# Optimization experiments

Measured on AMD Instinct MI355X. Metric: run time of the kernel, lower is better.

The kernel has to match this reference:

```python
import jax, jax.numpy as jnp
from jax import lax
import numpy as np

B, A, C = 8, 49104, 90
IMG = 512.0            # 512 + compound_coef*128, coef=0
SCORE_THR = 0.2
IOU_THR = 0.2
K_PRE = 1000           # top candidates kept before NMS (standard TF-style padded NMS)
K_OUT = 100            # max detections per image


def setup_inputs() -> dict:
    key = jax.random.key(0)
    k1, k2, k3, k4, k5, k6 = jax.random.split(key, 6)
    cls_preds = jax.random.uniform(k1, (B, A, C), dtype=jnp.float32)
    loc_preds = 0.1 * jax.random.normal(k2, (B, A, 4), dtype=jnp.float32)
    # plausible anchors in (y1, x1, y2, x2) within the 512x512 image
    cy = jax.random.uniform(k3, (A,)) * IMG
    cx = jax.random.uniform(k4, (A,)) * IMG
    h = 16.0 + jax.random.uniform(k5, (A,)) * 112.0
    w = 16.0 + jax.random.uniform(k6, (A,)) * 112.0
    anchors = jnp.stack([cy - h / 2, cx - w / 2, cy + h / 2, cx + w / 2], axis=-1).astype(jnp.float32)
    return {"cls_preds": cls_preds, "loc_preds": loc_preds, "anchors": anchors}


def _decode_and_clip(anchors, loc_preds):
    # anchors: [A,4] (y1,x1,y2,x2); loc_preds: [B,A,4] (dy,dx,dh,dw)
    ya = (anchors[:, 0] + anchors[:, 2]) / 2
    xa = (anchors[:, 1] + anchors[:, 3]) / 2
    ha = anchors[:, 2] - anchors[:, 0]
    wa = anchors[:, 3] - anchors[:, 1]
    dy, dx, dh, dw = loc_preds[..., 0], loc_preds[..., 1], loc_preds[..., 2], loc_preds[..., 3]
    h = jnp.exp(dh) * ha
    w = jnp.exp(dw) * wa
    yc = dy * ha + ya
    xc = dx * wa + xa
    # output boxes in (xmin, ymin, xmax, ymax), clipped to image
    boxes = jnp.stack([xc - w / 2, yc - h / 2, xc + w / 2, yc + h / 2], axis=-1)
    return jnp.clip(boxes, 0.0, IMG)


def _pairwise_iou(boxes):
    # boxes: [K,4] xyxy -> [K,K]
    x1 = jnp.maximum(boxes[:, None, 0], boxes[None, :, 0])
    y1 = jnp.maximum(boxes[:, None, 1], boxes[None, :, 1])
    x2 = jnp.minimum(boxes[:, None, 2], boxes[None, :, 2])
    y2 = jnp.minimum(boxes[:, None, 3], boxes[None, :, 3])
    inter = jnp.clip(x2 - x1, 0.0) * jnp.clip(y2 - y1, 0.0)
    area = (boxes[:, 2] - boxes[:, 0]) * (boxes[:, 3] - boxes[:, 1])
    return inter / (area[:, None] + area[None, :] - inter + 1e-8)


def _nms_single(scores, classes, boxes):
    # scores: [A], classes: [A] int32, boxes: [A,4]
    masked = jnp.where(scores > SCORE_THR, scores, -1.0)
    vals, idx = lax.top_k(masked, K_PRE)          # top candidates
    b = boxes[idx]                                 # [K_PRE,4]
    cls = classes[idx]                             # [K_PRE]
    # batched_nms trick: offset boxes per class so cross-class IoU is 0
    off = b + cls[:, None].astype(b.dtype) * (IMG + 1.0)
    ious = _pairwise_iou(off)                      # [K_PRE,K_PRE]

    def body(keep, i):
        sup = jnp.any(keep & (ious[:, i] > IOU_THR))
        k = (vals[i] > SCORE_THR) & (~sup)
        return keep.at[i].set(k), None

    keep, _ = lax.scan(body, jnp.zeros((K_PRE,), bool), jnp.arange(K_PRE))
    final = jnp.where(keep, vals, -1.0)
    fvals, fidx = lax.top_k(final, K_OUT)
    det = fvals > 0.0
    out_boxes = jnp.where(det[:, None], b[fidx], jnp.array([0.0, 0.0, 1.0, 1.0], dtype=b.dtype))
    out_scores = jnp.where(det, fvals, 0.0)
    out_labels = jnp.where(det, cls[fidx], -1)
    return out_boxes, out_scores, out_labels


def reference(cls_preds, loc_preds, anchors):
    boxes = _decode_and_clip(anchors, loc_preds)   # [B,A,4]
    scores = jnp.max(cls_preds, axis=2)            # [B,A]
    classes = jnp.argmax(cls_preds, axis=2).astype(jnp.int32)
    out_boxes, out_scores, out_labels = jax.vmap(_nms_single)(scores, classes, boxes)
    return out_boxes, out_scores, out_labels
```

## Files before the change

kernel.cpp:

```cpp
#include <hip/hip_runtime.h>
#include <stdint.h>

#define B_    8
#define A_    49104
#define C_    90
#define IMG_  512.0f
#define THR_  0.2f
#define KPRE  1000
#define KOUT  100
#define NCAND 1024
#define NKEY  2048
#define NBIN  1024
#define BINBASE 0x17C99u
#define THRU    0xBE4CCCCDu
#define GANCH 64
#define NBLKX ((A_ + GANCH - 1) / GANCH)
#define PREF_F 0.9997f

#define NPAD 1088
#define PADI(j) ((j) + ((j) >> 4))

static __device__ __forceinline__ uint32_t f2ord(float f) {
    uint32_t b = __float_as_uint(f);
    return (b & 0x80000000u) ? ~b : (b | 0x80000000u);
}
static __device__ __forceinline__ float ord2f(uint32_t u) {
    uint32_t b = (u & 0x80000000u) ? (u & 0x7FFFFFFFu) : ~u;
    return __uint_as_float(b);
}
static __device__ __forceinline__ uint64_t shflx64(uint64_t v, int m) {
    uint32_t lo = (uint32_t)v, hi = (uint32_t)(v >> 32);
    lo = (uint32_t)__shfl_xor((int)lo, m);
    hi = (uint32_t)__shfl_xor((int)hi, m);
    return ((uint64_t)hi << 32) | lo;
}

__global__ __launch_bounds__(256)
void k_score_compact(const float* __restrict__ cls,
                     uint32_t* __restrict__ scores_u,
                     uint64_t* __restrict__ blk_keys,
                     uint32_t* __restrict__ blk_cnt) {
    __shared__ float4 s4[(GANCH * C_) / 4];
    __shared__ float r_val[GANCH];
    __shared__ int   r_cls[GANCH];

    int tid = threadIdx.x;
    int b = blockIdx.y;
    int bx = blockIdx.x;
    int a0 = bx * GANCH;
    int valid = A_ - a0; if (valid > GANCH) valid = GANCH;

    const float4* src = (const float4*)(cls + (size_t)(b * A_ + a0) * C_);
    if (valid == GANCH) {
        float4 v0 = src[tid];
        float4 v1 = src[tid + 256];
        float4 v2 = src[tid + 512];
        float4 v3 = src[tid + 768];
        float4 v4 = src[tid + 1024];
        float4 v5;
        if (tid < 160) v5 = src[tid + 1280];
        s4[tid]        = v0;
        s4[tid + 256]  = v1;
        s4[tid + 512]  = v2;
        s4[tid + 768]  = v3;
        s4[tid + 1024] = v4;
        if (tid < 160) s4[tid + 1280] = v5;
    } else {
        int n4 = (valid * C_) / 4;
        for (int i = tid; i < n4; i += 256) s4[i] = src[i];
    }
    __syncthreads();

    const float* s = (const float*)s4;
    int g = tid >> 2, sub = tid & 3;
    float best = -1.0f; int bi = 0;
    if (g < valid) {
        #pragma unroll
        for (int j = sub; j < C_ + 2; j += 4) {
            if (j < C_) {
                float v = s[g * C_ + j];
                if (v > best) { best = v; bi = j; }
            }
        }
    }
    #pragma unroll
    for (int d = 1; d < 4; d <<= 1) {
        float ov = __shfl_xor(best, d);
        int   oi = __shfl_xor(bi, d);
        if (ov > best || (ov == best && oi < bi)) { best = ov; bi = oi; }
    }
    if (sub == 0 && g < valid) { r_val[g] = best; r_cls[g] = bi; }
    __syncthreads();

    if (tid < 64) {
        int a = a0 + tid;
        bool v = tid < valid;
        float bv = v ? r_val[tid] : -1.0f;
        if (v) {
            float m = (bv > THR_) ? bv : -1.0f;
            scores_u[b * A_ + a] = f2ord(m);
        }
        bool flag = v && (bv >= PREF_F);
        unsigned long long mb = __ballot(flag);
        if (flag) {
            int pos = (int)__popcll(mb & ((1ull << tid) - 1ull));
            uint64_t key = ((uint64_t)f2ord(bv) << 32)
                         | ((uint64_t)((~(uint32_t)a) & 0xFFFFu) << 16)
                         | ((uint64_t)(uint32_t)r_cls[tid] << 8);
            blk_keys[((size_t)(b * NBLKX + bx)) * GANCH + pos] = key;
        }
        if (tid == 0) blk_cnt[b * NBLKX + bx] = (uint32_t)__popcll(mb);
    }
}

__global__ __launch_bounds__(1024)
void k_seltop2(const uint32_t* __restrict__ scores_u,
               const float* __restrict__ cls,
               const float* __restrict__ loc,
               const float* __restrict__ anc,
               const uint64_t* __restrict__ blk_keys,
               const uint32_t* __restrict__ blk_cnt,
               float* __restrict__ cand_val,
               int* __restrict__ cand_cls,
               float* __restrict__ cand_box,
               int* __restrict__ n_valid) {
    int b = blockIdx.x;
    int t = threadIdx.x;
    __shared__ uint64_t keys[NKEY];
    __shared__ uint32_t pc[1024];
    __shared__ uint32_t sh_coarse;
    __shared__ int      sh_rem;
    __shared__ uint32_t sh_cutoff;
    __shared__ int      sh_cnt;
    const uint32_t* su = scores_u + (size_t)b * A_;

    uint32_t own = (t < NBLKX) ? blk_cnt[b * NBLKX + t] : 0u;
    pc[t] = own;
    __syncthreads();
    for (int d = 1; d < 1024; d <<= 1) {
        uint32_t v = (t >= d) ? pc[t - d] : 0u;
        __syncthreads();
        pc[t] += v;
        __syncthreads();
    }
    int n = (int)pc[1023];
    bool fast = (n >= KPRE && n <= NKEY);

    if (fast) {
        if (t < NBLKX && own) {
            int base = (int)pc[t] - (int)own;
            const uint64_t* src = blk_keys + ((size_t)(b * NBLKX + t)) * GANCH;
            for (int j = 0; j < (int)own; ++j) keys[base + j] = src[j];
        }
        for (int i = t; i < NKEY; i += 1024)
            if (i >= n) keys[i] = 0ull;
    } else {
        uint32_t* h = (uint32_t*)keys;
        h[t] = 0;
        if (t == 0) sh_cnt = 0;
        __syncthreads();
        for (int a = t; a < A_; a += 1024) {
            uint32_t u = su[a];
            if (u > THRU) {
                int bin = (int)(u >> 15) - (int)BINBASE;
                bin = bin < 0 ? 0 : (bin >= NBIN ? NBIN - 1 : bin);
                atomicAdd(&h[bin], 1u);
            }
        }
        __syncthreads();
        for (int d = 1; d < NBIN; d <<= 1) {
            uint32_t add = (t + d < NBIN) ? h[t + d] : 0u;
            __syncthreads();
            h[t] += add;
            __syncthreads();
        }
        {
            uint32_t St = h[t];
            uint32_t Sn = (t + 1 < NBIN) ? h[t + 1] : 0u;
            if (St >= KPRE && Sn < KPRE) {
                sh_coarse = (BINBASE + (uint32_t)t) << 15;
                sh_rem = KPRE - (int)Sn;
            }
            if (t == 0 && h[0] < KPRE) {
                sh_rem = 0;
                sh_coarse = 0xFFFFFFFFu;
                sh_cutoff = BINBASE << 15;
            }
        }
        __syncthreads();
        uint32_t coarse = sh_coarse;
        int rem = sh_rem;

        h[t] = 0;
        __syncthreads();
        if (rem > 0) {
            for (int a = t; a < A_; a += 1024) {
                uint32_t u = su[a];
                if ((u & 0xFFFF8000u) == coarse)
                    atomicAdd(&h[(u >> 5) & 0x3FF], 1u);
            }
        }
        __syncthreads();
        for (int d = 1; d < NBIN; d <<= 1) {
            uint32_t add = (t + d < NBIN) ? h[t + d] : 0u;
            __syncthreads();
            h[t] += add;
            __syncthreads();
        }
        if (rem > 0) {
            int St = (int)h[t];
            int Sn = (t + 1 < NBIN) ? (int)h[t + 1] : 0;
            if (St >= rem && Sn < rem)
                sh_cutoff = coarse | ((uint32_t)t << 5);
        }
        __syncthreads();
        uint32_t cutoff = sh_cutoff;
        __syncthreads();

        for (int a = t; a < A_; a += 1024) {
            uint32_t u = su[a];
            if (u >= cutoff) {
                int p = atomicAdd(&sh_cnt, 1);
                if (p < NKEY)
                    keys[p] = ((uint64_t)u << 32)
                            | ((uint64_t)((~(uint32_t)a) & 0xFFFFu) << 16);
            }
        }
        __syncthreads();
        n = sh_cnt; if (n > NKEY) n = NKEY;
        for (int i = t; i < NKEY; i += 1024)
            if (i >= n) keys[i] = 0ull;
    }
    __syncthreads();

    uint64_t x = keys[t], y = keys[t + 1024];
    for (int kk = 2; kk <= NKEY; kk <<= 1) {
        for (int jj = kk >> 1; jj > 0; jj >>= 1) {
            if (jj == 1024) {
                uint64_t mx = x > y ? x : y;
                uint64_t mn = x > y ? y : x;
                x = mx; y = mn;
                continue;
            }
            uint64_t px, py;
            if (jj >= 64) {
                keys[t] = x; keys[t + 1024] = y;
                __syncthreads();
                px = keys[t ^ jj]; py = keys[(t + 1024) ^ jj];
                __syncthreads();
            } else {
                px = shflx64(x, jj);
                py = shflx64(y, jj);
            }
            bool kmx = (((t & kk) == 0) == ((t & jj) == 0));
            x = kmx ? (x > px ? x : px) : (x > px ? px : x);
            int ty = t + 1024;
            bool kmy = (((ty & kk) == 0) == ((ty & jj) == 0));
            y = kmy ? (y > py ? y : py) : (y > py ? py : y);
        }
    }

    uint64_t key = x;
    bool real = (t < n);
    int ci = b * NCAND + t;
    if (real) {
        int a = (int)((~(uint32_t)(key >> 16)) & 0xFFFFu);
        int c;
        if (fast) {
            c = (int)((key >> 8) & 0xFFu);
        } else {
            const float* row = cls + ((size_t)b * A_ + a) * C_;
            float bb = -1.0f; int bc = 0;
            for (int j = 0; j < C_; ++j) { float q = row[j]; if (q > bb) { bb = q; bc = j; } }
            c = bc;
        }
        float4 an = ((const float4*)anc)[a];
        float4 l4 = ((const float4*)loc)[(size_t)b * A_ + a];
        float ya = (an.x + an.z) * 0.5f;
        float xa = (an.y + an.w) * 0.5f;
        float ha = an.z - an.x;
        float wa = an.w - an.y;
        float hh = expf(l4.z) * ha;
        float ww = expf(l4.w) * wa;
        float yc = l4.x * ha + ya;
        float xc = l4.y * wa + xa;
        float4 bx;
        bx.x = fminf(fmaxf(xc - ww * 0.5f, 0.0f), IMG_);
        bx.y = fminf(fmaxf(yc - hh * 0.5f, 0.0f), IMG_);
        bx.z = fminf(fmaxf(xc + ww * 0.5f, 0.0f), IMG_);
        bx.w = fminf(fmaxf(yc + hh * 0.5f, 0.0f), IMG_);
        cand_val[ci] = ord2f((uint32_t)(key >> 32));
        cand_cls[ci] = c;
        ((float4*)cand_box)[ci] = bx;
    } else {
        cand_val[ci] = -1.0f;
        cand_cls[ci] = 0;
        float4 z; z.x = z.y = z.z = z.w = 0.0f;
        ((float4*)cand_box)[ci] = z;
    }
    if (t == 0) n_valid[b] = n < KPRE ? n : KPRE;
}

__global__ void k_masks(const float* __restrict__ cand_box,
                        const int* __restrict__ cand_cls,
                        unsigned short* __restrict__ M16) {
    int b = blockIdx.x;
    __shared__ float x1s[NPAD], y1s[NPAD], x2s[NPAD], y2s[NPAD], ars[NPAD];
    for (int i = threadIdx.x; i < NCAND; i += blockDim.x) {
        int ci = b * NCAND + i;
        float4 bx = ((const float4*)cand_box)[ci];
        float off = (float)cand_cls[ci] * (IMG_ + 1.0f);
        float ox1 = bx.x + off, oy1 = bx.y + off;
        float ox2 = bx.z + off, oy2 = bx.w + off;
        int ip = PADI(i);
        x1s[ip] = ox1; y1s[ip] = oy1; x2s[ip] = ox2; y2s[ip] = oy2;
        ars[ip] = (ox2 - ox1) * (oy2 - oy1);
    }
    __syncthreads();

    int row0 = blockIdx.y * 63;
    for (int item = threadIdx.x; item < 63 * 64; item += blockDim.x) {
        int i = row0 + (item >> 6);
        if (i >= KPRE) continue;
        int w = item & 63;
        if (w < (i >> 4)) continue;
        int ip = PADI(i);
        float xi1 = x1s[ip], yi1 = y1s[ip], xi2 = x2s[ip], yi2 = y2s[ip], ai = ars[ip];
        unsigned int m = 0;
        int j0 = w * 16;
        #pragma unroll
        for (int q = 0; q < 16; ++q) {
            int jp = PADI(j0 + q);
            float xx1 = fmaxf(xi1, x1s[jp]);
            float yy1 = fmaxf(yi1, y1s[jp]);
            float xx2 = fminf(xi2, x2s[jp]);
            float yy2 = fminf(yi2, y2s[jp]);
            float iw = xx2 - xx1; iw = iw > 0.0f ? iw : 0.0f;
            float ih = yy2 - yy1; ih = ih > 0.0f ? ih : 0.0f;
            float inter = iw * ih;
            float den = (ai + ars[jp]) - inter + 1e-8f;
            float iou = inter / den;
            m |= (iou > THR_ ? 1u : 0u) << q;
        }
        M16[((size_t)(b * NCAND + i)) * 64 + w] = (unsigned short)m;
    }
}

__global__ void k_nms_out(const unsigned short* __restrict__ M16,
                          const float* __restrict__ cand_val,
                          const int* __restrict__ cand_cls,
                          const float* __restrict__ cand_box,
                          const int* __restrict__ n_valid,
                          float* __restrict__ out) {
    int b = blockIdx.x;
    int lane = threadIdx.x;
    int nv = n_valid[b]; if (nv > KPRE) nv = KPRE;
    const unsigned short* Mr = M16 + (size_t)b * NCAND * 64;
    __shared__ int kept[KOUT];

    uint32_t S = 0;
    int cnt = 0;
    uint32_t cur[8], nxt[8];
    #pragma unroll
    for (int t = 0; t < 8; ++t) cur[t] = Mr[(size_t)t * 64 + lane];

    for (int base = 0; base < nv && cnt < KOUT; base += 8) {
        #pragma unroll
        for (int t = 0; t < 8; ++t) {
            int r = base + 8 + t;
            nxt[t] = Mr[(size_t)(r < NCAND ? r : 0) * 64 + lane];
        }
        #pragma unroll
        for (int t = 0; t < 8; ++t) {
            int i = base + t;
            bool inb = (i < nv) && (cnt < KOUT);
            unsigned long long ball =
                __ballot(inb && (((S >> (i & 15)) & 1u) != 0u));
            int sup = (int)((ball >> (i >> 4)) & 1ull);
            if (inb && !sup) {
                S |= cur[t];
                if (lane == 0) kept[cnt] = i;
                cnt++;
            }
        }
        #pragma unroll
        for (int t = 0; t < 8; ++t) cur[t] = nxt[t];
    }
    __syncthreads();

    for (int s_ = lane; s_ < KOUT; s_ += 64) {
        float b0 = 0.0f, b1 = 0.0f, b2 = 1.0f, b3 = 1.0f, sc = 0.0f, lb = -1.0f;
        if (s_ < cnt) {
            int i = kept[s_];
            int ci = b * NCAND + i;
            float4 bx = ((const float4*)cand_box)[ci];
            b0 = bx.x; b1 = bx.y; b2 = bx.z; b3 = bx.w;
            sc = cand_val[ci];
            lb = (float)cand_cls[ci];
        }
        int ob = (b * KOUT + s_) * 4;
        out[ob + 0] = b0; out[ob + 1] = b1; out[ob + 2] = b2; out[ob + 3] = b3;
        out[B_ * KOUT * 4 + b * KOUT + s_] = sc;
        out[B_ * KOUT * 5 + b * KOUT + s_] = lb;
    }
}

extern "C" void kernel_launch(void* const* d_in, const int* in_sizes, int n_in,
                              void* d_out, int out_size, void* d_ws, size_t ws_size,
                              hipStream_t stream) {
    const float* cls = (const float*)d_in[0];
    const float* loc = (const float*)d_in[1];
    const float* anc = (const float*)d_in[2];
    float* out = (float*)d_out;

    char* ws = (char*)d_ws;
    size_t off = 0;
    auto alloc = [&](size_t bytes) -> void* {
        void* p = ws + off;
        off += (bytes + 255) & ~(size_t)255;
        return p;
    };
    uint32_t* scores_u = (uint32_t*)alloc((size_t)B_ * A_ * 4);
    uint64_t* blk_keys = (uint64_t*)alloc((size_t)B_ * NBLKX * GANCH * 8);
    uint32_t* blk_cnt  = (uint32_t*)alloc((size_t)B_ * NBLKX * 4);
    float*    cand_val = (float*)   alloc((size_t)B_ * NCAND * 4);
    int*      cand_cls = (int*)     alloc((size_t)B_ * NCAND * 4);
    float*    cand_box = (float*)   alloc((size_t)B_ * NCAND * 4 * 4);
    int*      n_valid  = (int*)     alloc((size_t)B_ * 4);
    unsigned short* M16 = (unsigned short*)alloc((size_t)B_ * NCAND * 64 * 2);

    dim3 gD(NBLKX, B_);
    k_score_compact<<<gD, 256, 0, stream>>>(cls, scores_u, blk_keys, blk_cnt);
    k_seltop2<<<B_, 1024, 0, stream>>>(
        scores_u, cls, loc, anc, blk_keys, blk_cnt,
        cand_val, cand_cls, cand_box, n_valid);
    k_masks<<<dim3(B_, 16), 256, 0, stream>>>(cand_box, cand_cls, M16);
    k_nms_out<<<B_, 64, 0, stream>>>(
        M16, cand_val, cand_cls, cand_box, n_valid, out);
}
```

Measured before the change: 269.8 us.

## Fuse top-k selection, IoU mask build and greedy NMS into one kernel

Merges the selection, IoU-mask and NMS-scan kernels into a single per-image 1024-thread block. Candidates stay in shared memory, and IoU masks are computed lazily in 64-row chunks that stop once 100 detections are kept. The block-level prefix sum is replaced with wave shuffles. This removes two launches and the global round-trip of the mask matrix, and can skip most mask work. In exchange, mask computation now runs on only 8 blocks instead of 128, and every chunk adds block-wide barriers.

Result: no change. 270.1 us (+0.1%).

```diff
diff --git a/kernel.cpp b/kernel.cpp
--- a/kernel.cpp
+++ b/kernel.cpp
@@ -19,6 +19,16 @@
 
 #define NPAD 1088
 #define PADI(j) ((j) + ((j) >> 4))
+
+#define OFF_X1   0
+#define OFF_Y1   4352
+#define OFF_X2   8704
+#define OFF_Y2   13056
+#define OFF_AR   17408
+#define OFF_MROW 21760
+#define OFF_KEPT 29952
+#define SMEM_SZ  30352
+#define OFF_WSUM 16384
 
 static __device__ __forceinline__ uint32_t f2ord(float f) {
     uint32_t b = __float_as_uint(f);
@@ -114,43 +124,64 @@
 }
 
 __global__ __launch_bounds__(1024)
-void k_seltop2(const uint32_t* __restrict__ scores_u,
-               const float* __restrict__ cls,
-               const float* __restrict__ loc,
-               const float* __restrict__ anc,
-               const uint64_t* __restrict__ blk_keys,
-               const uint32_t* __restrict__ blk_cnt,
-               float* __restrict__ cand_val,
-               int* __restrict__ cand_cls,
-               float* __restrict__ cand_box,
-               int* __restrict__ n_valid) {
+void k_select_nms(const uint32_t* __restrict__ scores_u,
+                  const float* __restrict__ cls,
+                  const float* __restrict__ loc,
+                  const float* __restrict__ anc,
+                  const uint64_t* __restrict__ blk_keys,
+                  const uint32_t* __restrict__ blk_cnt,
+                  float* __restrict__ cand_val,
+                  int* __restrict__ cand_cls,
+                  float* __restrict__ cand_box,
+                  float* __restrict__ out) {
     int b = blockIdx.x;
     int t = threadIdx.x;
-    __shared__ uint64_t keys[NKEY];
-    __shared__ uint32_t pc[1024];
+    __shared__ __align__(16) char smem[SMEM_SZ];
+    uint64_t* keys = (uint64_t*)smem;
+    uint32_t* wsum = (uint32_t*)(smem + OFF_WSUM);
+    float* x1s = (float*)(smem + OFF_X1);
+    float* y1s = (float*)(smem + OFF_Y1);
+    float* x2s = (float*)(smem + OFF_X2);
+    float* y2s = (float*)(smem + OFF_Y2);
+    float* ars = (float*)(smem + OFF_AR);
+    unsigned short* Mrow = (unsigned short*)(smem + OFF_MROW);
+    int* kept = (int*)(smem + OFF_KEPT);
     __shared__ uint32_t sh_coarse;
     __shared__ int      sh_rem;
     __shared__ uint32_t sh_cutoff;
     __shared__ int      sh_cnt;
+    __shared__ int      sh_kept;
     const uint32_t* su = scores_u + (size_t)b * A_;
 
+    int lane = t & 63, wv = t >> 6;
     uint32_t own = (t < NBLKX) ? blk_cnt[b * NBLKX + t] : 0u;
-    pc[t] = own;
-    __syncthreads();
-    for (int d = 1; d < 1024; d <<= 1) {
-        uint32_t v = (t >= d) ? pc[t - d] : 0u;
-        __syncthreads();
-        pc[t] += v;
-        __syncthreads();
-    }
-    int n = (int)pc[1023];
+    uint32_t v = own;
+    #pragma unroll
+    for (int d = 1; d < 64; d <<= 1) {
+        uint32_t u = (uint32_t)__shfl_up((int)v, d);
+        if (lane >= d) v += u;
+    }
+    if (lane == 63) wsum[wv] = v;
+    __syncthreads();
+    if (t < 16) {
+        uint32_t s = wsum[t];
+        #pragma unroll
+        for (int d = 1; d < 16; d <<= 1) {
+            uint32_t u = (uint32_t)__shfl_up((int)s, d);
+            if (t >= d) s += u;
+        }
+        wsum[t] = s;
+    }
+    __syncthreads();
+    int n = (int)wsum[15];
+    uint32_t incl = ((wv > 0) ? wsum[wv - 1] : 0u) + v;
     bool fast = (n >= KPRE && n <= NKEY);
 
     if (fast) {
         if (t < NBLKX && own) {
-            int base = (int)pc[t] - (int)own;
+            int base0 = (int)incl - (int)own;
             const uint64_t* src = blk_keys + ((size_t)(b * NBLKX + t)) * GANCH;
-            for (int j = 0; j < (int)own; ++j) keys[base + j] = src[j];
+            for (int j = 0; j < (int)own; ++j) keys[base0 + j] = src[j];
         }
         for (int i = t; i < NKEY; i += 1024)
             if (i >= n) keys[i] = 0ull;
@@ -259,13 +290,15 @@
             y = kmy ? (y > py ? y : py) : (y > py ? py : y);
         }
     }
+    __syncthreads();
 
     uint64_t key = x;
     bool real = (t < n);
     int ci = b * NCAND + t;
+    float4 bxo; bxo.x = bxo.y = bxo.z = bxo.w = 0.0f;
+    int c = 0; float val = -1.0f;
     if (real) {
         int a = (int)((~(uint32_t)(key >> 16)) & 0xFFFFu);
-        int c;
         if (fast) {
             c = (int)((key >> 8) & 0xFFu);
         } else {
@@ -284,119 +317,98 @@
         float ww = expf(l4.w) * wa;
         float yc = l4.x * ha + ya;
         float xc = l4.y * wa + xa;
-        float4 bx;
-        bx.x = fminf(fmaxf(xc - ww * 0.5f, 0.0f), IMG_);
-        bx.y = fminf(fmaxf(yc - hh * 0.5f, 0.0f), IMG_);
-        bx.z = fminf(fmaxf(xc + ww * 0.5f, 0.0f), IMG_);
-        bx.w = fminf(fmaxf(yc + hh * 0.5f, 0.0f), IMG_);
-        cand_val[ci] = ord2f((uint32_t)(key >> 32));
-        cand_cls[ci] = c;
-        ((float4*)cand_box)[ci] = bx;
-    } else {
-        cand_val[ci] = -1.0f;
-        cand_cls[ci] = 0;
-        float4 z; z.x = z.y = z.z = z.w = 0.0f;
-        ((float4*)cand_box)[ci] = z;
-    }
-    if (t == 0) n_valid[b] = n < KPRE ? n : KPRE;
-}
-
-__global__ void k_masks(const float* __restrict__ cand_box,
-                        const int* __restrict__ cand_cls,
-                        unsigned short* __restrict__ M16) {
-    int b = blockIdx.x;
-    __shared__ float x1s[NPAD], y1s[NPAD], x2s[NPAD], y2s[NPAD], ars[NPAD];
-    for (int i = threadIdx.x; i < NCAND; i += blockDim.x) {
-        int ci = b * NCAND + i;
-        float4 bx = ((const float4*)cand_box)[ci];
-        float off = (float)cand_cls[ci] * (IMG_ + 1.0f);
-        float ox1 = bx.x + off, oy1 = bx.y + off;
-        float ox2 = bx.z + off, oy2 = bx.w + off;
-        int ip = PADI(i);
+        bxo.x = fminf(fmaxf(xc - ww * 0.5f, 0.0f), IMG_);
+        bxo.y = fminf(fmaxf(yc - hh * 0.5f, 0.0f), IMG_);
+        bxo.z = fminf(fmaxf(xc + ww * 0.5f, 0.0f), IMG_);
+        bxo.w = fminf(fmaxf(yc + hh * 0.5f, 0.0f), IMG_);
+        val = ord2f((uint32_t)(key >> 32));
+    }
+    cand_val[ci] = val;
+    cand_cls[ci] = c;
+    ((float4*)cand_box)[ci] = bxo;
+    {
+        float off = (float)c * (IMG_ + 1.0f);
+        float ox1 = bxo.x + off, oy1 = bxo.y + off;
+        float ox2 = bxo.z + off, oy2 = bxo.w + off;
+        int ip = PADI(t);
         x1s[ip] = ox1; y1s[ip] = oy1; x2s[ip] = ox2; y2s[ip] = oy2;
         ars[ip] = (ox2 - ox1) * (oy2 - oy1);
     }
-    __syncthreads();
-
-    int row0 = blockIdx.y * 63;
-    for (int item = threadIdx.x; item < 63 * 64; item += blockDim.x) {
-        int i = row0 + (item >> 6);
-        if (i >= KPRE) continue;
-        int w = item & 63;
-        if (w < (i >> 4)) continue;
-        int ip = PADI(i);
-        float xi1 = x1s[ip], yi1 = y1s[ip], xi2 = x2s[ip], yi2 = y2s[ip], ai = ars[ip];
-        unsigned int m = 0;
-        int j0 = w * 16;
-        #pragma unroll
-        for (int q = 0; q < 16; ++q) {
-            int jp = PADI(j0 + q);
-            float xx1 = fmaxf(xi1, x1s[jp]);
-            float yy1 = fmaxf(yi1, y1s[jp]);
-            float xx2 = fminf(xi2, x2s[jp]);
-            float yy2 = fminf(yi2, y2s[jp]);
-            float iw = xx2 - xx1; iw = iw > 0.0f ? iw : 0.0f;
-            float ih = yy2 - yy1; ih = ih > 0.0f ? ih : 0.0f;
-            float inter = iw * ih;
-            float den = (ai + ars[jp]) - inter + 1e-8f;
-            float iou = inter / den;
-            m |= (iou > THR_ ? 1u : 0u) << q;
-        }
-        M16[((size_t)(b * NCAND + i)) * 64 + w] = (unsigned short)m;
-    }
-}
-
-__global__ void k_nms_out(const unsigned short* __restrict__ M16,
-                          const float* __restrict__ cand_val,
-                          const int* __restrict__ cand_cls,
-                          const float* __restrict__ cand_box,
-                          const int* __restrict__ n_valid,
-                          float* __restrict__ out) {
-    int b = blockIdx.x;
-    int lane = threadIdx.x;
-    int nv = n_valid[b]; if (nv > KPRE) nv = KPRE;
-    const unsigned short* Mr = M16 + (size_t)b * NCAND * 64;
-    __shared__ int kept[KOUT];
+    int nv = n < KPRE ? n : KPRE;
+    __syncthreads();
 
     uint32_t S = 0;
     int cnt = 0;
-    uint32_t cur[8], nxt[8];
-    #pragma unroll
-    for (int t = 0; t < 8; ++t) cur[t] = Mr[(size_t)t * 64 + lane];
-
-    for (int base = 0; base < nv && cnt < KOUT; base += 8) {
-        #pragma unroll
-        for (int t = 0; t < 8; ++t) {
-            int r = base + 8 + t;
-            nxt[t] = Mr[(size_t)(r < NCAND ? r : 0) * 64 + lane];
-        }
-        #pragma unroll
-        for (int t = 0; t < 8; ++t) {
-            int i = base + t;
-            bool inb = (i < nv) && (cnt < KOUT);
-            unsigned long long ball =
-                __ballot(inb && (((S >> (i & 15)) & 1u) != 0u));
-            int sup = (int)((ball >> (i >> 4)) & 1ull);
-            if (inb && !sup) {
-                S |= cur[t];
-                if (lane == 0) kept[cnt] = i;
-                cnt++;
-            }
-        }
-        #pragma unroll
-        for (int t = 0; t < 8; ++t) cur[t] = nxt[t];
-    }
-    __syncthreads();
-
-    for (int s_ = lane; s_ < KOUT; s_ += 64) {
+    int cnt_all = 0;
+    for (int base = 0; base < nv && cnt_all < KOUT; base += 64) {
+        for (int item = t; item < 64 * 64; item += 1024) {
+            int r = item >> 6;
+            int i = base + r;
+            if (i >= KPRE) continue;
+            int w = item & 63;
+            if (w < (i >> 4)) continue;
+            int ip = PADI(i);
+            float xi1 = x1s[ip], yi1 = y1s[ip], xi2 = x2s[ip], yi2 = y2s[ip], ai = ars[ip];
+            unsigned int m = 0;
+            int j0 = w * 16;
+            #pragma unroll
+            for (int q = 0; q < 16; ++q) {
+                int jp = PADI(j0 + q);
+                float xx1 = fmaxf(xi1, x1s[jp]);
+                float yy1 = fmaxf(yi1, y1s[jp]);
+                float xx2 = fminf(xi2, x2s[jp]);
+                float yy2 = fminf(yi2, y2s[jp]);
+                float iw = xx2 - xx1; iw = iw > 0.0f ? iw : 0.0f;
+                float ih = yy2 - yy1; ih = ih > 0.0f ? ih : 0.0f;
+                float inter = iw * ih;
+                float den = (ai + ars[jp]) - inter + 1e-8f;
+                float iou = inter / den;
+                m |= (iou > THR_ ? 1u : 0u) << q;
+            }
+            Mrow[r * 64 + w] = (unsigned short)m;
+        }
+        __syncthreads();
+        if (t < 64) {
+            uint32_t cur[8], nxt[8];
+            #pragma unroll
+            for (int q = 0; q < 8; ++q) cur[q] = Mrow[q * 64 + lane];
+            for (int g = 0; g < 8; ++g) {
+                #pragma unroll
+                for (int q = 0; q < 8; ++q) {
+                    int rn = (g + 1) * 8 + q;
+                    nxt[q] = Mrow[((rn < 64) ? rn : 0) * 64 + lane];
+                }
+                #pragma unroll
+                for (int q = 0; q < 8; ++q) {
+                    int i = base + g * 8 + q;
+                    bool inb = (i < nv) && (cnt < KOUT);
+                    unsigned long long ball =
+                        __ballot(inb && (((S >> (i & 15)) & 1u) != 0u));
+                    int sup = (int)((ball >> (i >> 4)) & 1ull);
+                    if (inb && !sup) {
+                        S |= cur[q];
+                        if (lane == 0) kept[cnt] = i;
+                        cnt++;
+                    }
+                }
+                #pragma unroll
+                for (int q = 0; q < 8; ++q) cur[q] = nxt[q];
+            }
+            if (t == 0) sh_kept = cnt;
+        }
+        __syncthreads();
+        cnt_all = sh_kept;
+    }
+
+    for (int s_ = t; s_ < KOUT; s_ += 1024) {
         float b0 = 0.0f, b1 = 0.0f, b2 = 1.0f, b3 = 1.0f, sc = 0.0f, lb = -1.0f;
-        if (s_ < cnt) {
+        if (s_ < cnt_all) {
             int i = kept[s_];
-            int ci = b * NCAND + i;
-            float4 bx = ((const float4*)cand_box)[ci];
+            int cj = b * NCAND + i;
+            float4 bx = ((const float4*)cand_box)[cj];
             b0 = bx.x; b1 = bx.y; b2 = bx.z; b3 = bx.w;
-            sc = cand_val[ci];
-            lb = (float)cand_cls[ci];
+            sc = cand_val[cj];
+            lb = (float)cand_cls[cj];
         }
         int ob = (b * KOUT + s_) * 4;
         out[ob + 0] = b0; out[ob + 1] = b1; out[ob + 2] = b2; out[ob + 3] = b3;
@@ -426,15 +438,10 @@
     float*    cand_val = (float*)   alloc((size_t)B_ * NCAND * 4);
     int*      cand_cls = (int*)     alloc((size_t)B_ * NCAND * 4);
     float*    cand_box = (float*)   alloc((size_t)B_ * NCAND * 4 * 4);
-    int*      n_valid  = (int*)     alloc((size_t)B_ * 4);
-    unsigned short* M16 = (unsigned short*)alloc((size_t)B_ * NCAND * 64 * 2);
 
     dim3 gD(NBLKX, B_);
     k_score_compact<<<gD, 256, 0, stream>>>(cls, scores_u, blk_keys, blk_cnt);
-    k_seltop2<<<B_, 1024, 0, stream>>>(
+    k_select_nms<<<B_, 1024, 0, stream>>>(
         scores_u, cls, loc, anc, blk_keys, blk_cnt,
-        cand_val, cand_cls, cand_box, n_valid);
-    k_masks<<<dim3(B_, 16), 256, 0, stream>>>(cand_box, cand_cls, M16);
-    k_nms_out<<<B_, 64, 0, stream>>>(
-        M16, cand_val, cand_cls, cand_box, n_valid, out);
-}
+        cand_val, cand_cls, cand_box, out);
+}
```
